# Kernel optimization log

Measured on AMD Instinct MI355X. Metric: run time of the kernel, lower is better.

Reference implementation:

```python
import jax, jax.numpy as jnp
import numpy as np

MAP_DS = 2.0
H, W = 512, 1024
MAXENT_WEIGHT = 1.0
EPS = 1e-5


def setup_inputs() -> dict:
    key = jax.random.key(0)
    k1, k2, k3 = jax.random.split(key, 3)
    B, T = 64, 256
    # Bounded random-walk trajectories in world coords (x in [0, H*ds), y in [0, W*ds))
    steps = jax.random.uniform(k1, (B, T, 2), minval=0.0, maxval=4.0)
    xy = jnp.cumsum(steps, axis=1) + 50.0
    xy = jnp.stack([jnp.clip(xy[..., 0], 0.0, H * MAP_DS - 1.0),
                    jnp.clip(xy[..., 1], 0.0, W * MAP_DS - 1.0)], axis=-1)
    # Pack into SE(2) pose matrices [B, T, 3, 3] with translation in [:2, 2]
    gt = jnp.tile(jnp.eye(3, dtype=jnp.float32), (B, T, 1, 1))
    gt = gt.at[:, :, 0, 2].set(xy[..., 0]).at[:, :, 1, 2].set(xy[..., 1])
    exp_svf = jax.random.uniform(k2, (B, H, W), dtype=jnp.float32)
    reward_preds = jax.random.normal(k3, (B, H, W), dtype=jnp.float32)
    return {"gt": gt, "exp_svf": exp_svf, "reward_preds": reward_preds}


def compute_expert_visitation(gt, max_steps):
    # gt: [B, T, 3, 3] SE(2) poses
    B = gt.shape[0]
    xy = gt[:, :, :2, 2] / MAP_DS                       # [B, T, 2] grid coords
    start = xy[:, :-1]                                  # [B, T-1, 2]
    end = xy[:, 1:]                                     # [B, T-1, 2]
    t = jnp.linspace(0.0, 1.0, max_steps, dtype=xy.dtype).reshape(1, 1, -1, 1)
    pts = start[:, :, None, :] + t * (end - start)[:, :, None, :]   # [B, T-1, S, 2]
    pts = pts.reshape(B, -1, 2)
    pts = jnp.concatenate([pts, xy[:, -1:]], axis=1)    # append last pose -> [B, N, 2]
    x = jnp.clip(pts[:, :, 0], 0, H - 1).astype(jnp.int32)
    y = jnp.clip(pts[:, :, 1], 0, W - 1).astype(jnp.int32)
    lin = x * W + y                                     # [B, N] flat indices
    flat = jnp.zeros((B, H * W), dtype=jnp.float32)
    flat = flat.at[jnp.arange(B)[:, None], lin].add(1.0)  # scatter-add histogram
    counts = jnp.minimum(flat, 1.0).reshape(B, H, W)      # binarize visitation
    return pts, counts


def reference(gt, exp_svf, reward_preds):
    # max_steps from concrete data, mirroring torch's .item() (eager, not traced)
    xy = np.asarray(gt)[:, :, :2, 2] / MAP_DS
    dist = np.linalg.norm(xy[:, 1:] - xy[:, :-1], axis=-1)
    max_steps = int(np.ceil(dist).max())
    interp_pts, svf = compute_expert_visitation(gt, max_steps)
    svf = svf / (svf.sum(axis=(1, 2), keepdims=True) + EPS)
    exp_svf = exp_svf / (exp_svf.sum(axis=(1, 2), keepdims=True) + EPS)
    svf_rewards = (svf * reward_preds).sum(axis=(1, 2))         # [B]
    exp_svf_rewards = (exp_svf * reward_preds).sum(axis=(1, 2))  # [B]
    visitation_loss = exp_svf_rewards.mean() - svf_rewards.mean()
    loss = MAXENT_WEIGHT * visitation_loss
    return loss, svf, interp_pts
```

## Files before the change

kernel.cpp:

```cpp
#include <hip/hip_runtime.h>

#define Bb 64
#define Tt 256
#define Hh 512
#define Ww 1024
#define HW (Hh * Ww)
#define EPSF 1e-5f

#define RB 2048
#define SB Bb

typedef float vf4 __attribute__((ext_vector_type(4)));


__device__ __forceinline__ void comp_pt(const float* __restrict__ gt, int b,
                                        int idx, int ms, int segN,
                                        float& px, float& py) {
    if (idx < segN) {
        int seg = idx / ms;
        int k = idx - seg * ms;
        const float* g0 = gt + (size_t)(b * Tt + seg) * 9;
        float sx = g0[2] * 0.5f, sy = g0[5] * 0.5f;
        float ex = g0[11] * 0.5f, ey = g0[14] * 0.5f;
        float t = (ms > 1) ? (float)k / (float)(ms - 1) : 0.0f;
        px = __fadd_rn(sx, __fmul_rn(t, __fsub_rn(ex, sx)));
        py = __fadd_rn(sy, __fmul_rn(t, __fsub_rn(ey, sy)));
    } else {
        const float* g0 = gt + (size_t)(b * Tt + (Tt - 1)) * 9;
        px = g0[2] * 0.5f;
        py = g0[5] * 0.5f;
    }
}

__device__ __forceinline__ int pt_cell(float px, float py) {
    int xi = (int)fminf(fmaxf(px, 0.0f), (float)(Hh - 1));
    int yi = (int)fminf(fmaxf(py, 0.0f), (float)(Ww - 1));
    return xi * Ww + yi;
}

__global__ __launch_bounds__(256) void combined_kernel(
        const float* __restrict__ exps, const float* __restrict__ rew,
        const float* __restrict__ gt,
        float* __restrict__ pts, float* __restrict__ svf,
        double* __restrict__ esum_p, double* __restrict__ edot_p,
        int* __restrict__ count_out, double* __restrict__ vdot_out,
        int ms, int P) {
    if (blockIdx.x < RB) {
        int b = blockIdx.x >> 5;
        int c = blockIdx.x & 31;
        size_t base = (size_t)b * HW + (size_t)c * 16384;

        float es = 0.0f, ed = 0.0f;
        #pragma unroll
        for (int j = 0; j < 2; ++j) {
            const vf4* e4 = (const vf4*)(exps + base) + j * 2048 + threadIdx.x;
            const vf4* r4 = (const vf4*)(rew  + base) + j * 2048 + threadIdx.x;
            vf4 ev[8], rv[8];
            #pragma unroll
            for (int k = 0; k < 8; ++k) ev[k] = e4[k * 256];
            #pragma unroll
            for (int k = 0; k < 8; ++k) rv[k] = r4[k * 256];
            #pragma unroll
            for (int k = 0; k < 8; ++k) {
                vf4 e = ev[k], r = rv[k];
                es += (e.x + e.y) + (e.z + e.w);
                ed += (e.x * r.x + e.y * r.y) + (e.z * r.z + e.w * r.w);
            }
        }

        for (int off = 32; off; off >>= 1) {
            es += __shfl_down(es, off);
            ed += __shfl_down(ed, off);
        }
        __shared__ float s_es[4], s_ed[4];
        int lane = threadIdx.x & 63, wv = threadIdx.x >> 6;
        if (lane == 0) { s_es[wv] = es; s_ed[wv] = ed; }
        __syncthreads();
        if (threadIdx.x == 0) {
            float tes = (s_es[0] + s_es[1]) + (s_es[2] + s_es[3]);
            float ted = (s_ed[0] + s_ed[1]) + (s_ed[2] + s_ed[3]);
            esum_p[blockIdx.x] = (double)tes;
            edot_p[blockIdx.x] = (double)ted;
        }
    } else {
        int b = blockIdx.x - RB;
        int segN = (Tt - 1) * ms;

        int myCount = 0;
        float myV = 0.0f;
        for (int idx = threadIdx.x; idx < P; idx += 256) {
            float px, py;
            comp_pt(gt, b, idx, ms, segN, px, py);
            size_t pi = ((size_t)b * P + idx) * 2;
            pts[pi]     = px;
            pts[pi + 1] = py;
            int cell = pt_cell(px, py);
            bool claim;
            if (idx == 0) {
                claim = true;
            } else {
                float qx, qy;
                comp_pt(gt, b, idx - 1, ms, segN, qx, qy);
                claim = (pt_cell(qx, qy) != cell);
            }
            if (claim) {
                myCount++;
                myV += rew[(size_t)b * HW + cell];
            }
        }

        for (int off = 32; off; off >>= 1) {
            myCount += __shfl_down(myCount, off);
            myV     += __shfl_down(myV, off);
        }
        __shared__ int   sc[4];
        __shared__ float sv[4];
        __shared__ float s_recip;
        int lane = threadIdx.x & 63, wv = threadIdx.x >> 6;
        if (lane == 0) { sc[wv] = myCount; sv[wv] = myV; }
        __syncthreads();
        if (threadIdx.x == 0) {
            int tot  = (sc[0] + sc[1]) + (sc[2] + sc[3]);
            float tv = (sv[0] + sv[1]) + (sv[2] + sv[3]);
            count_out[b] = tot;
            vdot_out[b]  = (double)tv;
            s_recip = 1.0f / ((float)tot + EPSF);
        }
        __syncthreads();
        float recip = s_recip;

        for (int idx = threadIdx.x; idx < P; idx += 256) {
            size_t pi = ((size_t)b * P + idx) * 2;
            float px = pts[pi], py = pts[pi + 1];
            svf[(size_t)b * HW + pt_cell(px, py)] = recip;
        }
    }
}

__global__ void loss_kernel(const double* __restrict__ esum_p,
                            const double* __restrict__ edot_p,
                            const double* __restrict__ vdot,
                            const int* __restrict__ count,
                            float* __restrict__ loss_out) {
    int b = threadIdx.x;
    double es = 0.0, ed = 0.0;
    #pragma unroll 8
    for (int c = 0; c < 32; ++c) {
        es += esum_p[b * 32 + c];
        ed += edot_p[b * 32 + c];
    }
    double e = ed / (es + 1e-5);
    double v = vdot[b] / ((double)count[b] + 1e-5);
    double term = e - v;
    for (int off = 32; off; off >>= 1) term += __shfl_down(term, off);
    if (b == 0) loss_out[0] = (float)(term / (double)Bb);
}

extern "C" void kernel_launch(void* const* d_in, const int* in_sizes, int n_in,
                              void* d_out, int out_size, void* d_ws, size_t ws_size,
                              hipStream_t stream) {
    const float* gt   = (const float*)d_in[0];
    const float* exps = (const float*)d_in[1];
    const float* rew  = (const float*)d_in[2];
    float* out = (float*)d_out;

    float* loss_out = out;
    float* svf = out + 1;
    int P  = (out_size - 1 - Bb * HW) / (Bb * 2);
    int ms = (P - 1) / (Tt - 1);
    float* pts = out + 1 + (size_t)Bb * HW;

    int*    count  = (int*)d_ws;
    double* vdot   = (double*)((char*)d_ws + 256);
    double* esum_p = (double*)((char*)d_ws + 768);
    double* edot_p = (double*)((char*)d_ws + 17152);

    hipMemsetAsync(svf, 0, (size_t)Bb * HW * sizeof(float), stream);

    combined_kernel<<<RB + SB, 256, 0, stream>>>(exps, rew, gt, pts, svf,
                                                 esum_p, edot_p, count, vdot,
                                                 ms, P);
    loss_kernel<<<1, 64, 0, stream>>>(esum_p, edot_p, vdot, count, loss_out);
}
```

Measured before the change: 338.4 us.

## Fuse svf zeroing into reduction blocks and scatter per chunk

Removes the separate hipMemsetAsync over the full svf buffer. Each reduction block now zeroes its own 16K-float chunk, recomputes the per-batch unique-cell count, and writes the reciprocal only into cells that fall inside its chunk. This saves a launch and lets the zero-fill overlap with the streaming reads. In exchange, every one of the 2048 blocks redundantly recomputes the trajectory points and the count over P, which adds ALU work and gt reads. The svf output is also misaligned by one float, so a head/tail path handles the unaligned edges.

```diff
diff --git a/kernel.cpp b/kernel.cpp
--- a/kernel.cpp
+++ b/kernel.cpp
@@ -7,8 +7,9 @@
 #define HW (Hh * Ww)
 #define EPSF 1e-5f
 
+#define SB Bb
 #define RB 2048
-#define SB Bb
+#define CHUNK 16384
 
 typedef float vf4 __attribute__((ext_vector_type(4)));
 
@@ -45,46 +46,10 @@
         double* __restrict__ esum_p, double* __restrict__ edot_p,
         int* __restrict__ count_out, double* __restrict__ vdot_out,
         int ms, int P) {
-    if (blockIdx.x < RB) {
-        int b = blockIdx.x >> 5;
-        int c = blockIdx.x & 31;
-        size_t base = (size_t)b * HW + (size_t)c * 16384;
-
-        float es = 0.0f, ed = 0.0f;
-        #pragma unroll
-        for (int j = 0; j < 2; ++j) {
-            const vf4* e4 = (const vf4*)(exps + base) + j * 2048 + threadIdx.x;
-            const vf4* r4 = (const vf4*)(rew  + base) + j * 2048 + threadIdx.x;
-            vf4 ev[8], rv[8];
-            #pragma unroll
-            for (int k = 0; k < 8; ++k) ev[k] = e4[k * 256];
-            #pragma unroll
-            for (int k = 0; k < 8; ++k) rv[k] = r4[k * 256];
-            #pragma unroll
-            for (int k = 0; k < 8; ++k) {
-                vf4 e = ev[k], r = rv[k];
-                es += (e.x + e.y) + (e.z + e.w);
-                ed += (e.x * r.x + e.y * r.y) + (e.z * r.z + e.w * r.w);
-            }
-        }
-
-        for (int off = 32; off; off >>= 1) {
-            es += __shfl_down(es, off);
-            ed += __shfl_down(ed, off);
-        }
-        __shared__ float s_es[4], s_ed[4];
-        int lane = threadIdx.x & 63, wv = threadIdx.x >> 6;
-        if (lane == 0) { s_es[wv] = es; s_ed[wv] = ed; }
-        __syncthreads();
-        if (threadIdx.x == 0) {
-            float tes = (s_es[0] + s_es[1]) + (s_es[2] + s_es[3]);
-            float ted = (s_ed[0] + s_ed[1]) + (s_ed[2] + s_ed[3]);
-            esum_p[blockIdx.x] = (double)tes;
-            edot_p[blockIdx.x] = (double)ted;
-        }
-    } else {
-        int b = blockIdx.x - RB;
-        int segN = (Tt - 1) * ms;
+    int segN = (Tt - 1) * ms;
+
+    if (blockIdx.x < SB) {
+        int b = blockIdx.x;
 
         int myCount = 0;
         float myV = 0.0f;
@@ -115,7 +80,6 @@
         }
         __shared__ int   sc[4];
         __shared__ float sv[4];
-        __shared__ float s_recip;
         int lane = threadIdx.x & 63, wv = threadIdx.x >> 6;
         if (lane == 0) { sc[wv] = myCount; sv[wv] = myV; }
         __syncthreads();
@@ -124,15 +88,83 @@
             float tv = (sv[0] + sv[1]) + (sv[2] + sv[3]);
             count_out[b] = tot;
             vdot_out[b]  = (double)tv;
-            s_recip = 1.0f / ((float)tot + EPSF);
-        }
+        }
+    } else {
+        int blk = blockIdx.x - SB;
+        int b = blk >> 5;
+        int c = blk & 31;
+        size_t base = (size_t)b * HW + (size_t)c * CHUNK;
+
+        {
+            float* p = svf + base;
+            int head = (int)((16 - ((uintptr_t)p & 15)) & 15) >> 2;
+            int nv   = (CHUNK - head) >> 2;
+            int tail = CHUNK - head - (nv << 2);
+            if ((int)threadIdx.x < head) p[threadIdx.x] = 0.0f;
+            if ((int)threadIdx.x < tail) p[head + (nv << 2) + threadIdx.x] = 0.0f;
+            vf4* v4 = (vf4*)(p + head);
+            vf4 z = {0.0f, 0.0f, 0.0f, 0.0f};
+            for (int k = (int)threadIdx.x; k < nv; k += 256) v4[k] = z;
+        }
+
+        float es = 0.0f, ed = 0.0f;
+        #pragma unroll
+        for (int j = 0; j < 2; ++j) {
+            const vf4* e4 = (const vf4*)(exps + base) + j * 2048 + threadIdx.x;
+            const vf4* r4 = (const vf4*)(rew  + base) + j * 2048 + threadIdx.x;
+            vf4 ev[8], rv[8];
+            #pragma unroll
+            for (int k = 0; k < 8; ++k) ev[k] = e4[k * 256];
+            #pragma unroll
+            for (int k = 0; k < 8; ++k) rv[k] = r4[k * 256];
+            #pragma unroll
+            for (int k = 0; k < 8; ++k) {
+                vf4 e = ev[k], r = rv[k];
+                es += (e.x + e.y) + (e.z + e.w);
+                ed += (e.x * r.x + e.y * r.y) + (e.z * r.z + e.w * r.w);
+            }
+        }
+        for (int off = 32; off; off >>= 1) {
+            es += __shfl_down(es, off);
+            ed += __shfl_down(ed, off);
+        }
+
+        int myCount = 0;
+        for (int idx = threadIdx.x; idx < P; idx += 256) {
+            float px, py;
+            comp_pt(gt, b, idx, ms, segN, px, py);
+            int cell = pt_cell(px, py);
+            bool claim;
+            if (idx == 0) {
+                claim = true;
+            } else {
+                float qx, qy;
+                comp_pt(gt, b, idx - 1, ms, segN, qx, qy);
+                claim = (pt_cell(qx, qy) != cell);
+            }
+            myCount += claim ? 1 : 0;
+        }
+        for (int off = 32; off; off >>= 1) myCount += __shfl_down(myCount, off);
+
+        __shared__ float s_es[4], s_ed[4];
+        __shared__ int   sc2[4];
+        int lane = threadIdx.x & 63, wv = threadIdx.x >> 6;
+        if (lane == 0) { s_es[wv] = es; s_ed[wv] = ed; sc2[wv] = myCount; }
         __syncthreads();
-        float recip = s_recip;
-
+        if (threadIdx.x == 0) {
+            esum_p[blk] = (double)((s_es[0] + s_es[1]) + (s_es[2] + s_es[3]));
+            edot_p[blk] = (double)((s_ed[0] + s_ed[1]) + (s_ed[2] + s_ed[3]));
+        }
+        int tot = (sc2[0] + sc2[1]) + (sc2[2] + sc2[3]);
+        float recip = 1.0f / ((float)tot + EPSF);
+
+        int lo = c * CHUNK, hi = lo + CHUNK;
         for (int idx = threadIdx.x; idx < P; idx += 256) {
-            size_t pi = ((size_t)b * P + idx) * 2;
-            float px = pts[pi], py = pts[pi + 1];
-            svf[(size_t)b * HW + pt_cell(px, py)] = recip;
+            float px, py;
+            comp_pt(gt, b, idx, ms, segN, px, py);
+            int cell = pt_cell(px, py);
+            if (cell >= lo && cell < hi)
+                svf[(size_t)b * HW + cell] = recip;
         }
     }
 }
@@ -175,9 +207,7 @@
     double* esum_p = (double*)((char*)d_ws + 768);
     double* edot_p = (double*)((char*)d_ws + 17152);
 
-    hipMemsetAsync(svf, 0, (size_t)Bb * HW * sizeof(float), stream);
-
-    combined_kernel<<<RB + SB, 256, 0, stream>>>(exps, rew, gt, pts, svf,
+    combined_kernel<<<SB + RB, 256, 0, stream>>>(exps, rew, gt, pts, svf,
                                                  esum_p, edot_p, count, vdot,
                                                  ms, P);
     loss_kernel<<<1, 64, 0, stream>>>(esum_p, edot_p, vdot, count, loss_out);
```

New measurement: 326.3 us. 1.04x faster.
